# Kernel optimization log

Hardware: AMD Instinct MI355X
Metric: run time of the kernel (lower is better)

Reference implementation:

```python
import jax, jax.numpy as jnp
import numpy as np

ITERATIONS = 3
EPS = 1e-06

def squash(s):
    # square_norm along last dim, keepdims (matches torch squash)
    sq = jnp.sum(s * s, axis=-1, keepdims=True)
    return sq / (1.0 + sq) * s / (jnp.sqrt(sq) + EPS)

def setup_inputs() -> dict:
    key = jax.random.key(0)
    k1, k2 = jax.random.split(key)
    x = jax.random.normal(k1, (64, 32, 8, 8, 16), dtype=jnp.float32)
    W = jax.random.normal(k2, (1, 32, 8, 8, 32, 16, 32), dtype=jnp.float32)
    return {"x": x, "W": W}

def reference(x, W):
    # u_hat: (B, C, H, Wd, O, D) = x (B,C,H,Wd,I) @ W (C,H,Wd,O,I,D)
    u_hat = jnp.einsum('bchwi,chwoid->bchwod', x, W[0])
    b = jnp.zeros(u_hat.shape[:-1], dtype=u_hat.dtype)  # (B,C,H,Wd,O)
    for _ in range(ITERATIONS - 1):
        c = jax.nn.softmax(b, axis=-1)
        s = jnp.sum(c[..., None] * u_hat, axis=(1, 2, 3))  # (B,O,D)
        v = squash(s)
        b = b + jnp.sum(u_hat * v[:, None, None, None], axis=-1)
    c = jax.nn.softmax(b, axis=-1)
    s = jnp.sum(c[..., None] * u_hat, axis=(1, 2, 3))
    return squash(s)  # (B, out_capsules, out_cap_dim)
```

## Files before the change

### kernel.cpp

```cpp
#include <hip/hip_runtime.h>
#include <math.h>

#define B_ 64
#define N_ 2048
#define O_ 32
#define I_ 16
#define D_ 32
#define OD_ 1024

typedef __attribute__((ext_vector_type(8))) short bf16x8;
typedef __attribute__((ext_vector_type(4))) float f32x4;

union FragU { unsigned u[4]; uint4 v; bf16x8 f; };

__device__ __forceinline__ void barrier_lds() {
  asm volatile("s_waitcnt lgkmcnt(0)\n\ts_barrier" ::: "memory");
}

template <int CTRL>
__device__ __forceinline__ float dpp_mov_f(float x) {
  return __int_as_float(
      __builtin_amdgcn_update_dpp(0, __float_as_int(x), CTRL, 0xf, 0xf, true));
}
__device__ __forceinline__ float row16_sum(float x) {
  x += dpp_mov_f<0x128>(x);
  x += dpp_mov_f<0x124>(x);
  x += dpp_mov_f<0x4e>(x);
  x += dpp_mov_f<0xb1>(x);
  return x;
}
__device__ __forceinline__ float grp32_max(float x) {
  x = fmaxf(x, dpp_mov_f<0xb1>(x));
  x = fmaxf(x, dpp_mov_f<0x4e>(x));
  x = fmaxf(x, dpp_mov_f<0x124>(x));
  x = fmaxf(x, dpp_mov_f<0x128>(x));
  x = fmaxf(x, __shfl_xor(x, 16));
  return x;
}
__device__ __forceinline__ float grp32_sum(float x) {
  x += dpp_mov_f<0xb1>(x);
  x += dpp_mov_f<0x4e>(x);
  x += dpp_mov_f<0x124>(x);
  x += dpp_mov_f<0x128>(x);
  x += __shfl_xor(x, 16);
  return x;
}

__device__ __forceinline__ void dk_split(float f, unsigned &h, unsigned &l) {
  unsigned u = __float_as_uint(f);
  h = u & 0xffff0000u;
  float lo = f - __uint_as_float(h);
  l = __float_as_uint(lo) >> 16;
}
__device__ __forceinline__ void dk_split16(float f, unsigned short &h,
                                           unsigned short &l) {
  unsigned u = __float_as_uint(f);
  unsigned hu = u & 0xffff0000u;
  h = (unsigned short)(u >> 16);
  float lo = f - __uint_as_float(hu);
  l = (unsigned short)(__float_as_uint(lo) >> 16);
}
__device__ __forceinline__ unsigned pk(unsigned short e0, unsigned short e1) {
  return (unsigned)e0 | ((unsigned)e1 << 16);
}

__global__ __launch_bounds__(256) void prep_all(const float* __restrict__ W,
                                                const float* __restrict__ x,
                                                uint4* __restrict__ WP,
                                                uint4* __restrict__ XP) {
  __shared__ float tile[8 * 512];
  const int tid = threadIdx.x;
  if (blockIdx.x < 8192) {
    const int pair0 = blockIdx.x * 8;
    const f32x4* gsrc = (const f32x4*)(W + (size_t)pair0 * 512);
    f32x4* lds4 = (f32x4*)tile;
#pragma unroll
    for (int k = 0; k < 4; ++k)
      lds4[tid + k * 256] = __builtin_nontemporal_load(gsrc + tid + k * 256);
    __syncthreads();
    const int p = tid >> 5;
    const int d = tid & 31;
    const int pair = pair0 + p;
    unsigned short hh[I_], ll[I_];
#pragma unroll
    for (int i = 0; i < I_; ++i)
      dk_split16(tile[p * 512 + i * 32 + d], hh[i], ll[i]);
    const int c = d & 15, dhalf = d >> 4;
    size_t base = ((size_t)pair * 2 + dhalf) * 4;
#pragma unroll
    for (int sel = 0; sel < 2; ++sel) {
      const unsigned short* e = sel ? ll : hh;
#pragma unroll
      for (int qp = 0; qp < 2; ++qp) {
        uint4 u;
        u.x = pk(e[qp * 8 + 0], e[qp * 8 + 1]);
        u.y = pk(e[qp * 8 + 2], e[qp * 8 + 3]);
        u.z = pk(e[qp * 8 + 4], e[qp * 8 + 5]);
        u.w = pk(e[qp * 8 + 6], e[qp * 8 + 7]);
        WP[(base + sel * 2 + qp) * 16 + c] = u;
      }
    }
  } else {
    int t = (blockIdx.x - 8192) * 256 + tid;
    int c = t & 15, n = (t >> 4) & 2047, bg = t >> 15;
    const f32x4* xq = (const f32x4*)(x + ((size_t)(bg * 16 + c) * N_ + n) * I_);
    float xv[I_];
#pragma unroll
    for (int k = 0; k < 4; ++k) {
      f32x4 q4 = __builtin_nontemporal_load(xq + k);
      xv[4 * k + 0] = q4[0];
      xv[4 * k + 1] = q4[1];
      xv[4 * k + 2] = q4[2];
      xv[4 * k + 3] = q4[3];
    }
    unsigned short hh[I_], ll[I_];
#pragma unroll
    for (int i = 0; i < I_; ++i) dk_split16(xv[i], hh[i], ll[i]);
    size_t base = ((size_t)bg * N_ + n) * 4;
#pragma unroll
    for (int sel = 0; sel < 2; ++sel) {
      const unsigned short* e = sel ? ll : hh;
#pragma unroll
      for (int qp = 0; qp < 2; ++qp) {
        uint4 u;
        u.x = pk(e[qp * 8 + 0], e[qp * 8 + 1]);
        u.y = pk(e[qp * 8 + 2], e[qp * 8 + 3]);
        u.z = pk(e[qp * 8 + 4], e[qp * 8 + 5]);
        u.w = pk(e[qp * 8 + 6], e[qp * 8 + 7]);
        XP[(base + sel * 2 + qp) * 16 + c] = u;
      }
    }
  }
}

template <int UNIFORM>
__global__ __launch_bounds__(1024, 4) void mfma_pass6(
    const uint4* __restrict__ XP, const uint4* __restrict__ WP,
    const float* __restrict__ v, float* __restrict__ partial, int NC) {
  const int tid = threadIdx.x;
  const int lane = tid & 63;
  const int w = tid >> 6;
  const int q = lane >> 4;
  const int c = lane & 15;
  const int qp = q & 1;
  const int ch = blockIdx.x;
  const int bgy = blockIdx.y;

  __shared__ uint4 xps[2][16][4][16];
  __shared__ float ls_logit[32 * O_];
  __shared__ float ls_c[32 * O_];

  const int n0 = ch * NC;

  {
    uint4* xf = (uint4*)xps;
    const int total = 2 * NC * 64;
    for (int l = tid; l < total; l += 1024) {
      int bgl = l / (NC * 64);
      int rest = l - bgl * (NC * 64);
      xf[bgl * 1024 + rest] =
          XP[(size_t)(bgy * 2 + bgl) * 131072 + (size_t)n0 * 64 + rest];
    }
  }

  f32x4 s_t[2][4];
#pragma unroll
  for (int bgl = 0; bgl < 2; ++bgl)
#pragma unroll
    for (int ct = 0; ct < 4; ++ct) s_t[bgl][ct] = (f32x4){0.f, 0.f, 0.f, 0.f};

  float vreg[2][4][4];
  if (!UNIFORM) {
#pragma unroll
    for (int bgl = 0; bgl < 2; ++bgl)
#pragma unroll
      for (int ct = 0; ct < 4; ++ct) {
        int odc = (2 * w + (ct >> 1)) * 32 + (ct & 1) * 16 + c;
#pragma unroll
        for (int r = 0; r < 4; ++r)
          vreg[bgl][ct][r] =
              v[(size_t)(bgy * 32 + bgl * 16 + q * 4 + r) * OD_ + odc];
      }
  }

  barrier_lds();

  const uint4* wbase = WP + (size_t)(2 * w) * 128 + lane;

  FragU cb[4];
#pragma unroll
  for (int ct = 0; ct < 4; ++ct)
    cb[ct].v = wbase[(size_t)n0 * 4096 + ct * 64];

  for (int nl = 0; nl < NC; ++nl) {
    const size_t n = (size_t)(n0 + nl);
    const size_t np = (nl + 1 < NC) ? n + 1 : n;
    FragU cbn[4];

    if (UNIFORM) {
#pragma unroll
      for (int ct = 0; ct < 4; ++ct) cbn[ct].v = wbase[np * 4096 + ct * 64];
#pragma unroll
      for (int bgl = 0; bgl < 2; ++bgl) {
        FragU ah, al;
        ah.v = xps[bgl][nl][qp][c];
        al.v = xps[bgl][nl][2 + qp][c];
#pragma unroll
        for (int ct = 0; ct < 4; ++ct) {
          s_t[bgl][ct] = __builtin_amdgcn_mfma_f32_16x16x32_bf16(
              ah.f, cb[ct].f, s_t[bgl][ct], 0, 0, 0);
          s_t[bgl][ct] = __builtin_amdgcn_mfma_f32_16x16x32_bf16(
              al.f, cb[ct].f, s_t[bgl][ct], 0, 0, 0);
        }
      }
    } else {
#pragma unroll
      for (int bgl = 0; bgl < 2; ++bgl) {
        FragU ah, al;
        ah.v = xps[bgl][nl][qp][c];
        al.v = xps[bgl][nl][2 + qp][c];
        float lg[2][4];
#pragma unroll
        for (int ol = 0; ol < 2; ++ol)
#pragma unroll
          for (int r = 0; r < 4; ++r) lg[ol][r] = 0.f;
#pragma unroll
        for (int ct = 0; ct < 4; ++ct) {
          f32x4 acc = (f32x4){0.f, 0.f, 0.f, 0.f};
          acc = __builtin_amdgcn_mfma_f32_16x16x32_bf16(ah.f, cb[ct].f, acc, 0, 0, 0);
          f32x4 u = __builtin_amdgcn_mfma_f32_16x16x32_bf16(al.f, cb[ct].f, acc, 0, 0, 0);
          int ol = ct >> 1;
#pragma unroll
          for (int r = 0; r < 4; ++r)
            lg[ol][r] = fmaf(u[r], vreg[bgl][ct][r], lg[ol][r]);
        }
#pragma unroll
        for (int ol = 0; ol < 2; ++ol)
#pragma unroll
          for (int r = 0; r < 4; ++r) lg[ol][r] = row16_sum(lg[ol][r]);
        if (c == 0) {
#pragma unroll
          for (int ol = 0; ol < 2; ++ol)
#pragma unroll
            for (int r = 0; r < 4; ++r)
              ls_logit[(bgl * 16 + q * 4 + r) * O_ + 2 * w + ol] = lg[ol][r];
        }
      }
#pragma unroll
      for (int ct = 0; ct < 4; ++ct) cbn[ct].v = wbase[np * 4096 + ct * 64];

      barrier_lds();
      {
        float l = ls_logit[tid];
        float mx = grp32_max(l);
        float e = __expf(l - mx);
        float sm = grp32_sum(e);
        ls_c[tid] = e / sm;
      }
      barrier_lds();
#pragma unroll
      for (int bgl = 0; bgl < 2; ++bgl) {
        FragU ah, al;
        ah.v = xps[bgl][nl][qp][c];
        al.v = xps[bgl][nl][2 + qp][c];
#pragma unroll
        for (int ct = 0; ct < 4; ++ct) {
          f32x4 acc = (f32x4){0.f, 0.f, 0.f, 0.f};
          acc = __builtin_amdgcn_mfma_f32_16x16x32_bf16(ah.f, cb[ct].f, acc, 0, 0, 0);
          f32x4 u = __builtin_amdgcn_mfma_f32_16x16x32_bf16(al.f, cb[ct].f, acc, 0, 0, 0);
          int o = 2 * w + (ct >> 1);
#pragma unroll
          for (int r = 0; r < 4; ++r) {
            float cc = ls_c[(bgl * 16 + q * 4 + r) * O_ + o];
            s_t[bgl][ct][r] = fmaf(cc, u[r], s_t[bgl][ct][r]);
          }
        }
      }
    }
#pragma unroll
    for (int ct = 0; ct < 4; ++ct) cb[ct] = cbn[ct];
  }

  const float scale = UNIFORM ? (1.f / 32.f) : 1.f;
#pragma unroll
  for (int bgl = 0; bgl < 2; ++bgl)
#pragma unroll
    for (int ct = 0; ct < 4; ++ct) {
      int odc = (2 * w + (ct >> 1)) * 32 + (ct & 1) * 16 + c;
#pragma unroll
      for (int r = 0; r < 4; ++r) {
        partial[((size_t)ch * B_ + bgy * 32 + bgl * 16 + q * 4 + r) * OD_ + odc] =
            s_t[bgl][ct][r] * scale;
      }
    }
}

template <int UNIFORM>
__global__ __launch_bounds__(512, 4) void mfma_pass_fb(
    const float* __restrict__ x, const float* __restrict__ W,
    const float* __restrict__ v, float* __restrict__ partial, int NC) {
  const int tid = threadIdx.x;
  const int lane = tid & 63;
  const int cg = tid >> 6;
  const int q = lane >> 4;
  const int c = lane & 15;
  const int ch = blockIdx.x;
  const int bg = blockIdx.y;

  __shared__ float ls_logit[16 * O_];
  __shared__ float ls_c[16 * O_];

  f32x4 s_t[8];
#pragma unroll
  for (int ct = 0; ct < 8; ++ct) s_t[ct] = (f32x4){0.f, 0.f, 0.f, 0.f};

  const int n0 = ch * NC;
  const int ih = (q & 1) * 8;
  const float* xrow = x + ((size_t)(bg * 16 + c) * N_) * I_ + ih;

  for (int nl = 0; nl < NC; ++nl) {
    const int n = n0 + nl;
    const float* xp = xrow + (size_t)n * I_;
    float4 xv0 = *(const float4*)xp;
    float4 xv1 = *(const float4*)(xp + 4);
    float xv[8] = {xv0.x, xv0.y, xv0.z, xv0.w, xv1.x, xv1.y, xv1.z, xv1.w};
    FragU a1;
#pragma unroll
    for (int p = 0; p < 4; ++p) {
      unsigned h0, l0, h1, l1;
      dk_split(xv[2 * p], h0, l0);
      dk_split(xv[2 * p + 1], h1, l1);
      a1.u[p] = (q < 2) ? ((h0 >> 16) | h1) : (l0 | (l1 << 16));
    }
    f32x4 u_t[8];
#pragma unroll
    for (int ct = 0; ct < 8; ++ct) {
      const int o = cg * 4 + (ct >> 1);
      const int d = (ct & 1) * 16 + c;
      const float* wp = W + (((size_t)n * O_ + o) * I_ + ih) * D_ + d;
      FragU b1, b2;
#pragma unroll
      for (int p = 0; p < 4; ++p) {
        unsigned h0, l0, h1, l1;
        dk_split(wp[(2 * p) * D_], h0, l0);
        dk_split(wp[(2 * p + 1) * D_], h1, l1);
        b1.u[p] = (h0 >> 16) | h1;
        b2.u[p] = l0 | (l1 << 16);
      }
      if (UNIFORM) {
        s_t[ct] = __builtin_amdgcn_mfma_f32_16x16x32_bf16(a1.f, b1.f, s_t[ct], 0, 0, 0);
        s_t[ct] = __builtin_amdgcn_mfma_f32_16x16x32_bf16(a1.f, b2.f, s_t[ct], 0, 0, 0);
      } else {
        f32x4 acc = (f32x4){0.f, 0.f, 0.f, 0.f};
        acc = __builtin_amdgcn_mfma_f32_16x16x32_bf16(a1.f, b1.f, acc, 0, 0, 0);
        u_t[ct] = __builtin_amdgcn_mfma_f32_16x16x32_bf16(a1.f, b2.f, acc, 0, 0, 0);
      }
    }
    if (!UNIFORM) {
#pragma unroll
      for (int ol = 0; ol < 4; ++ol) {
        float lg[4] = {0.f, 0.f, 0.f, 0.f};
#pragma unroll
        for (int hf = 0; hf < 2; ++hf) {
          int ct = ol * 2 + hf;
          int odc = cg * 128 + ct * 16 + c;
#pragma unroll
          for (int r = 0; r < 4; ++r)
            lg[r] = fmaf(u_t[ct][r], v[(size_t)(bg * 16 + q * 4 + r) * OD_ + odc], lg[r]);
        }
#pragma unroll
        for (int r = 0; r < 4; ++r) {
#pragma unroll
          for (int m = 1; m < 16; m <<= 1) lg[r] += __shfl_xor(lg[r], m);
        }
        if (c == 0) {
#pragma unroll
          for (int r = 0; r < 4; ++r)
            ls_logit[(q * 4 + r) * O_ + cg * 4 + ol] = lg[r];
        }
      }
      __syncthreads();
      {
        int b_l = tid >> 5, o = tid & 31;
        float l = ls_logit[b_l * O_ + o];
        float mx = l;
#pragma unroll
        for (int m = 16; m >= 1; m >>= 1) mx = fmaxf(mx, __shfl_xor(mx, m));
        float e = __expf(l - mx);
        float sm = e;
#pragma unroll
        for (int m = 16; m >= 1; m >>= 1) sm += __shfl_xor(sm, m);
        ls_c[b_l * O_ + o] = e / sm;
      }
      __syncthreads();
#pragma unroll
      for (int ol = 0; ol < 4; ++ol) {
        int o = cg * 4 + ol;
        float cc[4];
#pragma unroll
        for (int r = 0; r < 4; ++r) cc[r] = ls_c[(q * 4 + r) * O_ + o];
#pragma unroll
        for (int hf = 0; hf < 2; ++hf) {
          int ct = ol * 2 + hf;
#pragma unroll
          for (int r = 0; r < 4; ++r)
            s_t[ct][r] = fmaf(cc[r], u_t[ct][r], s_t[ct][r]);
        }
      }
    }
  }

  const float scale = UNIFORM ? (1.f / 32.f) : 1.f;
#pragma unroll
  for (int ct = 0; ct < 8; ++ct) {
#pragma unroll
    for (int r = 0; r < 4; ++r) {
      partial[((size_t)ch * B_ + bg * 16 + q * 4 + r) * OD_ + cg * 128 + ct * 16 + c] =
          s_t[ct][r] * scale;
    }
  }
}

__global__ __launch_bounds__(256) void reduce_fused(
    const float4* __restrict__ part, int cq4, const float4* __restrict__ prev,
    float4* __restrict__ out) {
  __shared__ float4 accs[4][64];
  const int lane = threadIdx.x & 63;
  const int cg = threadIdx.x >> 6;
  const int g4 = blockIdx.x * 64 + lane;
  float4 s = make_float4(0.f, 0.f, 0.f, 0.f);
  const int c0 = cg * cq4;
  for (int i = 0; i < cq4; ++i) {
    float4 p = part[(size_t)(c0 + i) * 16384 + g4];
    s.x += p.x; s.y += p.y; s.z += p.z; s.w += p.w;
  }
  accs[cg][lane] = s;
  __syncthreads();
  if (cg == 0) {
    float4 a1 = accs[1][lane], a2 = accs[2][lane], a3 = accs[3][lane];
    s.x += a1.x + a2.x + a3.x;
    s.y += a1.y + a2.y + a3.y;
    s.z += a1.z + a2.z + a3.z;
    s.w += a1.w + a2.w + a3.w;
    float sq = s.x * s.x + s.y * s.y + s.z * s.z + s.w * s.w;
#pragma unroll
    for (int m = 4; m >= 1; m >>= 1) sq += __shfl_xor(sq, m, 8);
    float scale = sq / ((1.f + sq) * (sqrtf(sq) + 1e-6f));
    float4 r = make_float4(s.x * scale, s.y * scale, s.z * scale, s.w * scale);
    if (prev) {
      float4 p = prev[g4];
      r.x += p.x; r.y += p.y; r.z += p.z; r.w += p.w;
    }
    out[g4] = r;
  }
}

__global__ __launch_bounds__(256) void reduce_squash(
    const float4* __restrict__ part, int chunks,
    const float4* __restrict__ prev, float4* __restrict__ out) {
  int g4 = blockIdx.x * 256 + threadIdx.x;
  float4 s = make_float4(0.f, 0.f, 0.f, 0.f);
#pragma unroll 4
  for (int ch = 0; ch < chunks; ++ch) {
    float4 p = part[(size_t)ch * 16384 + g4];
    s.x += p.x; s.y += p.y; s.z += p.z; s.w += p.w;
  }
  float sq = s.x * s.x + s.y * s.y + s.z * s.z + s.w * s.w;
#pragma unroll
  for (int m = 4; m >= 1; m >>= 1) sq += __shfl_xor(sq, m, 8);
  float scale = sq / ((1.f + sq) * (sqrtf(sq) + 1e-6f));
  float4 r = make_float4(s.x * scale, s.y * scale, s.z * scale, s.w * scale);
  if (prev) {
    float4 p = prev[g4];
    r.x += p.x; r.y += p.y; r.z += p.z; r.w += p.w;
  }
  out[g4] = r;
}

extern "C" void kernel_launch(void* const* d_in, const int* in_sizes, int n_in,
                              void* d_out, int out_size, void* d_ws,
                              size_t ws_size, hipStream_t stream) {
  const float* x = (const float*)d_in[0];
  const float* W = (const float*)d_in[1];
  float* out = (float*)d_out;

  const size_t XP_FLOATS = 4ull * 2048 * 4 * 16 * 4;
  const size_t WP_FLOATS = 2048ull * 32 * 2 * 4 * 16 * 4;

  float* v1 = (float*)d_ws;
  float* vsum = v1 + 65536;
  float* partial = vsum + 65536;

  const int chunks = 128;
  bool packed_path =
      (131072 + (size_t)chunks * 65536 + XP_FLOATS + WP_FLOATS) * 4 <= ws_size;

  if (packed_path) {
    uint4* XP = (uint4*)(partial + (size_t)chunks * 65536);
    uint4* WP = XP + XP_FLOATS / 4;
    const int NC = N_ / chunks;
    const int cq4 = chunks / 4;
    dim3 grid(chunks, 2);

    prep_all<<<8704, 256, 0, stream>>>(W, x, WP, XP);

    mfma_pass6<1><<<grid, 1024, 0, stream>>>(XP, WP, nullptr, partial, NC);
    reduce_fused<<<256, 256, 0, stream>>>((const float4*)partial, cq4, nullptr,
                                          (float4*)v1);
    mfma_pass6<0><<<grid, 1024, 0, stream>>>(XP, WP, v1, partial, NC);
    reduce_fused<<<256, 256, 0, stream>>>((const float4*)partial, cq4,
                                          (const float4*)v1, (float4*)vsum);
    mfma_pass6<0><<<grid, 1024, 0, stream>>>(XP, WP, vsum, partial, NC);
    reduce_fused<<<256, 256, 0, stream>>>((const float4*)partial, cq4, nullptr,
                                          (float4*)out);
  } else {
    int fchunks = 128;
    while (fchunks > 1 && (131072 + (size_t)fchunks * 65536) * 4 > ws_size)
      fchunks >>= 1;
    int NC = N_ / fchunks;
    dim3 grid(fchunks, 4);

    mfma_pass_fb<1><<<grid, 512, 0, stream>>>(x, W, nullptr, partial, NC);
    reduce_squash<<<64, 256, 0, stream>>>((const float4*)partial, fchunks,
                                          nullptr, (float4*)v1);
    mfma_pass_fb<0><<<grid, 512, 0, stream>>>(x, W, v1, partial, NC);
    reduce_squash<<<64, 256, 0, stream>>>((const float4*)partial, fchunks,
                                          (const float4*)v1, (float4*)vsum);
    mfma_pass_fb<0><<<grid, 512, 0, stream>>>(x, W, vsum, partial, NC);
    reduce_squash<<<64, 256, 0, stream>>>((const float4*)partial, fchunks,
                                          nullptr, (float4*)out);
  }
}
```

Before: 377.3 us.

## Batch routing softmax over eight capsule positions to cut barriers

Measured after the change: 408.1 us. +8.2%, slower.

```diff
diff --git a/kernel.cpp b/kernel.cpp
--- a/kernel.cpp
+++ b/kernel.cpp
@@ -147,8 +147,7 @@
   const int bgy = blockIdx.y;
 
   __shared__ uint4 xps[2][16][4][16];
-  __shared__ float ls_logit[32 * O_];
-  __shared__ float ls_c[32 * O_];
+  __shared__ float ls_sm[8 * 32 * O_];
 
   const int n0 = ch * NC;
 
@@ -192,12 +191,11 @@
   for (int ct = 0; ct < 4; ++ct)
     cb[ct].v = wbase[(size_t)n0 * 4096 + ct * 64];
 
-  for (int nl = 0; nl < NC; ++nl) {
-    const size_t n = (size_t)(n0 + nl);
-    const size_t np = (nl + 1 < NC) ? n + 1 : n;
-    FragU cbn[4];
-
-    if (UNIFORM) {
+  if (UNIFORM) {
+    for (int nl = 0; nl < NC; ++nl) {
+      const size_t n = (size_t)(n0 + nl);
+      const size_t np = (nl + 1 < NC) ? n + 1 : n;
+      FragU cbn[4];
 #pragma unroll
       for (int ct = 0; ct < 4; ++ct) cbn[ct].v = wbase[np * 4096 + ct * 64];
 #pragma unroll
@@ -213,72 +211,105 @@
               al.f, cb[ct].f, s_t[bgl][ct], 0, 0, 0);
         }
       }
-    } else {
-#pragma unroll
-      for (int bgl = 0; bgl < 2; ++bgl) {
-        FragU ah, al;
-        ah.v = xps[bgl][nl][qp][c];
-        al.v = xps[bgl][nl][2 + qp][c];
-        float lg[2][4];
-#pragma unroll
-        for (int ol = 0; ol < 2; ++ol)
-#pragma unroll
-          for (int r = 0; r < 4; ++r) lg[ol][r] = 0.f;
-#pragma unroll
-        for (int ct = 0; ct < 4; ++ct) {
-          f32x4 acc = (f32x4){0.f, 0.f, 0.f, 0.f};
-          acc = __builtin_amdgcn_mfma_f32_16x16x32_bf16(ah.f, cb[ct].f, acc, 0, 0, 0);
-          f32x4 u = __builtin_amdgcn_mfma_f32_16x16x32_bf16(al.f, cb[ct].f, acc, 0, 0, 0);
-          int ol = ct >> 1;
-#pragma unroll
-          for (int r = 0; r < 4; ++r)
-            lg[ol][r] = fmaf(u[r], vreg[bgl][ct][r], lg[ol][r]);
-        }
-#pragma unroll
-        for (int ol = 0; ol < 2; ++ol)
-#pragma unroll
-          for (int r = 0; r < 4; ++r) lg[ol][r] = row16_sum(lg[ol][r]);
-        if (c == 0) {
+#pragma unroll
+      for (int ct = 0; ct < 4; ++ct) cb[ct] = cbn[ct];
+    }
+  } else {
+    for (int s2 = 0; s2 < 2; ++s2) {
+      const int nb = s2 * 8;
+#pragma unroll 2
+      for (int j = 0; j < 8; ++j) {
+        const int nl = nb + j;
+        const size_t n = (size_t)(n0 + nl);
+        const size_t np = (j < 7) ? n + 1 : (size_t)(n0 + nb);
+        FragU cbn[4];
+#pragma unroll
+        for (int ct = 0; ct < 4; ++ct) cbn[ct].v = wbase[np * 4096 + ct * 64];
+#pragma unroll
+        for (int bgl = 0; bgl < 2; ++bgl) {
+          FragU ah, al;
+          ah.v = xps[bgl][nl][qp][c];
+          al.v = xps[bgl][nl][2 + qp][c];
+          float lg[2][4];
 #pragma unroll
           for (int ol = 0; ol < 2; ++ol)
 #pragma unroll
+            for (int r = 0; r < 4; ++r) lg[ol][r] = 0.f;
+#pragma unroll
+          for (int ct = 0; ct < 4; ++ct) {
+            f32x4 acc = (f32x4){0.f, 0.f, 0.f, 0.f};
+            acc = __builtin_amdgcn_mfma_f32_16x16x32_bf16(ah.f, cb[ct].f, acc, 0, 0, 0);
+            f32x4 u = __builtin_amdgcn_mfma_f32_16x16x32_bf16(al.f, cb[ct].f, acc, 0, 0, 0);
+            int ol = ct >> 1;
+#pragma unroll
             for (int r = 0; r < 4; ++r)
-              ls_logit[(bgl * 16 + q * 4 + r) * O_ + 2 * w + ol] = lg[ol][r];
-        }
-      }
-#pragma unroll
-      for (int ct = 0; ct < 4; ++ct) cbn[ct].v = wbase[np * 4096 + ct * 64];
-
+              lg[ol][r] = fmaf(u[r], vreg[bgl][ct][r], lg[ol][r]);
+          }
+#pragma unroll
+          for (int ol = 0; ol < 2; ++ol)
+#pragma unroll
+            for (int r = 0; r < 4; ++r) lg[ol][r] = row16_sum(lg[ol][r]);
+          if (c == 0) {
+#pragma unroll
+            for (int ol = 0; ol < 2; ++ol)
+#pragma unroll
+              for (int r = 0; r < 4; ++r)
+                ls_sm[j * 1024 + (bgl * 16 + q * 4 + r) * O_ + 2 * w + ol] =
+                    lg[ol][r];
+          }
+        }
+#pragma unroll
+        for (int ct = 0; ct < 4; ++ct) cb[ct] = cbn[ct];
+      }
       barrier_lds();
-      {
-        float l = ls_logit[tid];
-        float mx = grp32_max(l);
-        float e = __expf(l - mx);
-        float sm = grp32_sum(e);
-        ls_c[tid] = e / sm;
+#pragma unroll
+      for (int g = 0; g < 2; ++g) {
+        float l[4], mx[4], e[4], sm[4];
+#pragma unroll
+        for (int jj = 0; jj < 4; ++jj) l[jj] = ls_sm[(g * 4 + jj) * 1024 + tid];
+#pragma unroll
+        for (int jj = 0; jj < 4; ++jj) mx[jj] = grp32_max(l[jj]);
+#pragma unroll
+        for (int jj = 0; jj < 4; ++jj) e[jj] = __expf(l[jj] - mx[jj]);
+#pragma unroll
+        for (int jj = 0; jj < 4; ++jj) sm[jj] = grp32_sum(e[jj]);
+#pragma unroll
+        for (int jj = 0; jj < 4; ++jj)
+          ls_sm[(g * 4 + jj) * 1024 + tid] = e[jj] / sm[jj];
       }
       barrier_lds();
-#pragma unroll
-      for (int bgl = 0; bgl < 2; ++bgl) {
-        FragU ah, al;
-        ah.v = xps[bgl][nl][qp][c];
-        al.v = xps[bgl][nl][2 + qp][c];
-#pragma unroll
-        for (int ct = 0; ct < 4; ++ct) {
-          f32x4 acc = (f32x4){0.f, 0.f, 0.f, 0.f};
-          acc = __builtin_amdgcn_mfma_f32_16x16x32_bf16(ah.f, cb[ct].f, acc, 0, 0, 0);
-          f32x4 u = __builtin_amdgcn_mfma_f32_16x16x32_bf16(al.f, cb[ct].f, acc, 0, 0, 0);
-          int o = 2 * w + (ct >> 1);
-#pragma unroll
-          for (int r = 0; r < 4; ++r) {
-            float cc = ls_c[(bgl * 16 + q * 4 + r) * O_ + o];
-            s_t[bgl][ct][r] = fmaf(cc, u[r], s_t[bgl][ct][r]);
+#pragma unroll 2
+      for (int j = 0; j < 8; ++j) {
+        const int nl = nb + j;
+        const size_t n = (size_t)(n0 + nl);
+        const size_t np = (j < 7) ? n + 1
+                                  : (s2 == 0 ? (size_t)(n0 + 8) : n);
+        FragU cbn[4];
+#pragma unroll
+        for (int ct = 0; ct < 4; ++ct) cbn[ct].v = wbase[np * 4096 + ct * 64];
+#pragma unroll
+        for (int bgl = 0; bgl < 2; ++bgl) {
+          FragU ah, al;
+          ah.v = xps[bgl][nl][qp][c];
+          al.v = xps[bgl][nl][2 + qp][c];
+#pragma unroll
+          for (int ct = 0; ct < 4; ++ct) {
+            f32x4 acc = (f32x4){0.f, 0.f, 0.f, 0.f};
+            acc = __builtin_amdgcn_mfma_f32_16x16x32_bf16(ah.f, cb[ct].f, acc, 0, 0, 0);
+            f32x4 u = __builtin_amdgcn_mfma_f32_16x16x32_bf16(al.f, cb[ct].f, acc, 0, 0, 0);
+            int o = 2 * w + (ct >> 1);
+#pragma unroll
+            for (int r = 0; r < 4; ++r) {
+              float cc = ls_sm[j * 1024 + (bgl * 16 + q * 4 + r) * O_ + o];
+              s_t[bgl][ct][r] = fmaf(cc, u[r], s_t[bgl][ct][r]);
+            }
           }
         }
-      }
-    }
-#pragma unroll
-    for (int ct = 0; ct < 4; ++ct) cb[ct] = cbn[ct];
+#pragma unroll
+        for (int ct = 0; ct < 4; ++ct) cb[ct] = cbn[ct];
+      }
+      barrier_lds();
+    }
   }
 
   const float scale = UNIFORM ? (1.f / 32.f) : 1.f;
```
